# Performance work log

Measured on AMD Instinct MI355X. Metric: run time of the kernel, lower is better.

The kernel has to match this reference:

```python
import jax, jax.numpy as jnp
import numpy as np
from jax import lax

SIZE = 3
BETA = 0.95
THRESH = 1.0
NUM_STEPS = 25
B = 32768


def setup_inputs() -> dict:
    key = jax.random.key(0)
    ks = jax.random.split(key, 9)
    x = jax.random.uniform(ks[0], (B, SIZE, SIZE), dtype=jnp.float32)
    def lin(k, out_d, in_d):
        kw, kb = jax.random.split(k)
        s = 1.0 / np.sqrt(in_d)
        W = jax.random.uniform(kw, (out_d, in_d), minval=-s, maxval=s, dtype=jnp.float32)
        b = jax.random.uniform(kb, (out_d,), minval=-s, maxval=s, dtype=jnp.float32)
        return W, b
    W1, b1 = lin(ks[1], 30, 3)
    W2, b2 = lin(ks[2], 30, 30)
    W3, b3 = lin(ks[3], 3, 30)
    W4, b4 = lin(ks[4], 2, 3)
    return {"x": x, "W1": W1, "b1": b1, "W2": W2, "b2": b2,
            "W3": W3, "b3": b3, "W4": W4, "b4": b4}


def _forward(x, W1, b1, W2, b2, W3, b3, W4, b4):
    b = x.shape[0]
    xf = x.reshape(b, SIZE * SIZE)  # [B, 9]

    # snntorch Leaky (subtract reset, threshold=1): reset uses previous mem's spike.
    def step(mem, _):
        reset = (mem > THRESH).astype(xf.dtype)
        mem_new = BETA * mem + xf - reset * THRESH
        spk = (mem_new > THRESH).astype(xf.dtype)
        return mem_new, spk

    mem0 = jnp.zeros_like(xf)
    _, spks = lax.scan(step, mem0, None, length=NUM_STEPS)  # [T, B, 9]

    grid = spks.reshape(NUM_STEPS, b, SIZE, SIZE)           # [T, B, 3, 3]
    cols = jnp.swapaxes(grid, -1, -2)
    lines = jnp.concatenate([grid, cols], axis=2)            # [T, B, 6, 3]

    h = jax.nn.relu(jnp.einsum('tbls,hs->tblh', lines, W1) + b1)  # [T,B,6,30]
    h = jax.nn.relu(jnp.einsum('tblh,gh->tblg', h, W2) + b2)      # [T,B,6,30]
    h = jax.nn.relu(jnp.einsum('tblg,sg->tbls', h, W3) + b3)      # [T,B,6,3]
    h = jax.nn.relu(jnp.einsum('tbls,os->tblo', h, W4) + b4)      # [T,B,6,2]
    p = jax.nn.softmax(h, axis=-1)  # Softmax(dim=0) on a 1-D size-2 vector
    # sum over the 6 line predictions per step, then over the 25 timesteps
    return p.sum(axis=(0, 2))  # [B, 2]


def reference(x, W1, b1, W2, b2, W3, b3, W4, b4):
    return _forward(x, W1, b1, W2, b2, W3, b3, W4, b4)
```

## Files before the change

### kernel.cpp

```cpp
#include <hip/hip_runtime.h>

#define NUM_STEPS 25
#define THREADS 256

__global__ __launch_bounds__(THREADS) void snn_lut_kernel(
    const float* __restrict__ x,
    const float* __restrict__ W1, const float* __restrict__ b1,
    const float* __restrict__ W2, const float* __restrict__ b2,
    const float* __restrict__ W3, const float* __restrict__ b3,
    const float* __restrict__ W4, const float* __restrict__ b4,
    float* __restrict__ out, int B)
{
    __shared__ float h1s[8][30];
    __shared__ float h2s[8][32];
    __shared__ float h3s[8][3];
    __shared__ float2 lut[8];

    const int tid = threadIdx.x;

    if (tid < 240) {
        const int p = tid / 30, h = tid % 30;
        const float i0 = (float)(p & 1);
        const float i1 = (float)((p >> 1) & 1);
        const float i2 = (float)((p >> 2) & 1);
        float v = W1[h * 3 + 0] * i0 + W1[h * 3 + 1] * i1 + W1[h * 3 + 2] * i2 + b1[h];
        h1s[p][h] = fmaxf(v, 0.0f);
    }
    __syncthreads();
    if (tid < 240) {
        const int p = tid / 30, h = tid % 30;
        float v = b2[h];
        #pragma unroll
        for (int k = 0; k < 30; ++k) v += W2[h * 30 + k] * h1s[p][k];
        h2s[p][h] = fmaxf(v, 0.0f);
    }
    __syncthreads();
    if (tid < 24) {
        const int p = tid / 3, h = tid % 3;
        float v = b3[h];
        #pragma unroll
        for (int k = 0; k < 30; ++k) v += W3[h * 30 + k] * h2s[p][k];
        h3s[p][h] = fmaxf(v, 0.0f);
    }
    __syncthreads();
    if (tid < 8) {
        const int p = tid;
        float o0 = b4[0], o1 = b4[1];
        #pragma unroll
        for (int k = 0; k < 3; ++k) {
            o0 += W4[0 * 3 + k] * h3s[p][k];
            o1 += W4[1 * 3 + k] * h3s[p][k];
        }
        o0 = fmaxf(o0, 0.0f);
        o1 = fmaxf(o1, 0.0f);
        const float e0 = expf(o0), e1 = expf(o1);
        const float inv = 1.0f / (e0 + e1);
        lut[p] = make_float2(e0 * inv, e1 * inv);
    }
    __syncthreads();

    const int b = blockIdx.x * THREADS + tid;
    if (b >= B) return;

    float xv[9], m[9];
    #pragma unroll
    for (int c = 0; c < 9; ++c) {
        xv[c] = x[b * 9 + c];
        m[c] = 0.0f;
    }

    float acc0 = 0.0f, acc1 = 0.0f;
    for (int t = 0; t < NUM_STEPS; ++t) {
        int s[9];
        #pragma unroll
        for (int c = 0; c < 9; ++c) {
            const float r = (m[c] > 1.0f) ? 1.0f : 0.0f;
            m[c] = __fsub_rn(__fadd_rn(__fmul_rn(0.95f, m[c]), xv[c]), r);
            s[c] = (m[c] > 1.0f) ? 1 : 0;
        }
        const int p0 = s[0] | (s[1] << 1) | (s[2] << 2);
        const int p1 = s[3] | (s[4] << 1) | (s[5] << 2);
        const int p2 = s[6] | (s[7] << 1) | (s[8] << 2);
        const int p3 = s[0] | (s[3] << 1) | (s[6] << 2);
        const int p4 = s[1] | (s[4] << 1) | (s[7] << 2);
        const int p5 = s[2] | (s[5] << 1) | (s[8] << 2);

        const float2 l0 = lut[p0], l1 = lut[p1], l2 = lut[p2];
        const float2 l3 = lut[p3], l4 = lut[p4], l5 = lut[p5];
        acc0 += l0.x + l1.x + l2.x + l3.x + l4.x + l5.x;
        acc1 += l0.y + l1.y + l2.y + l3.y + l4.y + l5.y;
    }

    out[b * 2 + 0] = acc0;
    out[b * 2 + 1] = acc1;
}

extern "C" void kernel_launch(void* const* d_in, const int* in_sizes, int n_in,
                              void* d_out, int out_size, void* d_ws, size_t ws_size,
                              hipStream_t stream) {
    const float* x  = (const float*)d_in[0];
    const float* W1 = (const float*)d_in[1];
    const float* b1 = (const float*)d_in[2];
    const float* W2 = (const float*)d_in[3];
    const float* b2 = (const float*)d_in[4];
    const float* W3 = (const float*)d_in[5];
    const float* b3 = (const float*)d_in[6];
    const float* W4 = (const float*)d_in[7];
    const float* b4 = (const float*)d_in[8];
    float* out = (float*)d_out;

    const int B = in_sizes[0] / 9;
    const int blocks = (B + THREADS - 1) / THREADS;
    snn_lut_kernel<<<blocks, THREADS, 0, stream>>>(
        x, W1, b1, W2, b2, W3, b3, W4, b4, out, B);
}
```

Before: 77.36 us.

## Count LUT pattern occurrences in packed histogram, overlap with LUT build, stage x in LDS

Each thread now packs the 150 per-step pattern hits into a 64-bit histogram of 8-bit counters instead of doing LUT lookups and float adds every step. The LUT is read only once at the end to form weighted sums, and the final barrier moves after the time loop so the spiking recurrence overlaps with the MLP LUT construction. Input x is loaded into shared memory with coalesced strided loads, and the output is written as float2. The change alters the float summation order, and the x staging loop has no bounds check for a partial last block.

```diff
diff --git a/kernel.cpp b/kernel.cpp
--- a/kernel.cpp
+++ b/kernel.cpp
@@ -15,8 +15,19 @@
     __shared__ float h2s[8][32];
     __shared__ float h3s[8][3];
     __shared__ float2 lut[8];
+    __shared__ float xs[THREADS * 9];
 
     const int tid = threadIdx.x;
+    const int blk0 = blockIdx.x * THREADS;
+
+    {
+        const float* xb = x + (size_t)blk0 * 9;
+        #pragma unroll
+        for (int k = 0; k < 9; ++k) {
+            const int i = tid + k * THREADS;
+            xs[i] = xb[i];
+        }
+    }
 
     if (tid < 240) {
         const int p = tid / 30, h = tid % 30;
@@ -57,26 +68,24 @@
         const float inv = 1.0f / (e0 + e1);
         lut[p] = make_float2(e0 * inv, e1 * inv);
     }
-    __syncthreads();
 
-    const int b = blockIdx.x * THREADS + tid;
-    if (b >= B) return;
-
-    float xv[9], m[9];
+    float xv[9], m[9], r[9];
     #pragma unroll
     for (int c = 0; c < 9; ++c) {
-        xv[c] = x[b * 9 + c];
+        xv[c] = xs[tid * 9 + c];
         m[c] = 0.0f;
+        r[c] = 0.0f;
     }
 
-    float acc0 = 0.0f, acc1 = 0.0f;
+    unsigned long long hist = 0ULL;
     for (int t = 0; t < NUM_STEPS; ++t) {
         int s[9];
         #pragma unroll
         for (int c = 0; c < 9; ++c) {
-            const float r = (m[c] > 1.0f) ? 1.0f : 0.0f;
-            m[c] = __fsub_rn(__fadd_rn(__fmul_rn(0.95f, m[c]), xv[c]), r);
-            s[c] = (m[c] > 1.0f) ? 1 : 0;
+            m[c] = __fsub_rn(__fadd_rn(__fmul_rn(0.95f, m[c]), xv[c]), r[c]);
+            const bool sp = m[c] > 1.0f;
+            s[c] = sp ? 1 : 0;
+            r[c] = sp ? 1.0f : 0.0f;
         }
         const int p0 = s[0] | (s[1] << 1) | (s[2] << 2);
         const int p1 = s[3] | (s[4] << 1) | (s[5] << 2);
@@ -85,14 +94,25 @@
         const int p4 = s[1] | (s[4] << 1) | (s[7] << 2);
         const int p5 = s[2] | (s[5] << 1) | (s[8] << 2);
 
-        const float2 l0 = lut[p0], l1 = lut[p1], l2 = lut[p2];
-        const float2 l3 = lut[p3], l4 = lut[p4], l5 = lut[p5];
-        acc0 += l0.x + l1.x + l2.x + l3.x + l4.x + l5.x;
-        acc1 += l0.y + l1.y + l2.y + l3.y + l4.y + l5.y;
+        hist += (1ULL << (p0 << 3)) + (1ULL << (p1 << 3)) + (1ULL << (p2 << 3))
+              + (1ULL << (p3 << 3)) + (1ULL << (p4 << 3)) + (1ULL << (p5 << 3));
     }
 
-    out[b * 2 + 0] = acc0;
-    out[b * 2 + 1] = acc1;
+    __syncthreads();
+
+    float acc0 = 0.0f, acc1 = 0.0f;
+    #pragma unroll
+    for (int p = 0; p < 8; ++p) {
+        const float cnt = (float)((hist >> (p << 3)) & 0xFFULL);
+        const float2 l = lut[p];
+        acc0 += cnt * l.x;
+        acc1 += cnt * l.y;
+    }
+
+    const int b = blk0 + tid;
+    if (b < B) {
+        reinterpret_cast<float2*>(out)[b] = make_float2(acc0, acc1);
+    }
 }
 
 extern "C" void kernel_launch(void* const* d_in, const int* in_sizes, int n_in,
```

Measured after the change: 75.48 us. 1.02x faster.
